# Kernel optimization log

Hardware: AMD Instinct MI355X
Metric: run time of the kernel (lower is better)

Reference implementation:

```python
import jax, jax.numpy as jnp
import numpy as np

NEG = -100000.0  # matches torch masked_fill constant

def setup_inputs() -> dict:
    key = jax.random.key(0)
    k1, k2, k3, k4 = jax.random.split(key, 4)
    B, T, D, H, S = 8, 2048, 1024, 8, 128
    features = jax.random.normal(k1, (B, T, D), dtype=jnp.float32)
    begins = jax.random.randint(k2, (B, S), 0, 2016, dtype=jnp.int64)
    widths = jax.random.randint(k3, (B, S), 1, 33, dtype=jnp.int64)
    ends = jnp.minimum(begins + widths, T)
    key_w = jax.random.normal(k4, (H, D), dtype=jnp.float32) / np.sqrt(D)
    key_b = jnp.zeros((H,), dtype=jnp.float32)
    return {"features": features, "begins": begins, "ends": ends,
            "key_w": key_w, "key_b": key_b}


def reference(features, begins, ends, key_w, key_b):
    # features: [B, T, D]; begins/ends: [B, S]
    B, T, D = features.shape
    H = key_w.shape[0]
    S = begins.shape[1]
    pos = jnp.arange(T)  # [T]
    # span mask [B, S, T]
    mask = (begins[..., None] <= pos) & (pos < ends[..., None])
    # key projection: [B, T, H]
    logits = jnp.einsum('btd,hd->bth', features, key_w) + key_b
    # masked softmax over T per (batch, span, head): [B, S, T, H]
    masked = jnp.where(mask[..., None], logits[:, None, :, :], NEG)
    weights = jax.nn.softmax(masked, axis=-2)
    # values = features reshaped to heads: [B, T, H, D//H]
    values = features.reshape(B, T, H, D // H)
    res = jnp.einsum('bthd,bsth->bshd', values, weights)  # [B, S, H, D//H]
    return res.reshape(B, S, D)
```

## Files before the change

kernel.cpp:

```cpp
#include <hip/hip_runtime.h>

#define B_  8
#define T_  2048
#define D_  1024
#define H_  8
#define S_  128
#define DH_ 128
#define MAXW 32

__global__ __launch_bounds__(256) void logits_kernel(
    const float* __restrict__ feat,
    const float* __restrict__ kw,
    const float* __restrict__ kb,
    float* __restrict__ logits)
{
    const int wave = threadIdx.x >> 6;
    const int lane = threadIdx.x & 63;
    const int row  = blockIdx.x * 4 + wave;

    const float* fr = feat + (size_t)row * D_;
    float4 f[4];
#pragma unroll
    for (int c = 0; c < 4; ++c)
        f[c] = *(const float4*)(fr + c * 256 + lane * 4);

    float acc[H_];
#pragma unroll
    for (int h = 0; h < H_; ++h) {
        const float* kr = kw + h * D_;
        float s = 0.f;
#pragma unroll
        for (int c = 0; c < 4; ++c) {
            float4 k = *(const float4*)(kr + c * 256 + lane * 4);
            s += f[c].x * k.x + f[c].y * k.y + f[c].z * k.z + f[c].w * k.w;
        }
        acc[h] = s;
    }

#pragma unroll
    for (int off = 32; off >= 1; off >>= 1) {
#pragma unroll
        for (int h = 0; h < H_; ++h)
            acc[h] += __shfl_xor(acc[h], off, 64);
    }

    if (lane == 0) {
        float4 o0 = make_float4(acc[0] + kb[0], acc[1] + kb[1],
                                acc[2] + kb[2], acc[3] + kb[3]);
        float4 o1 = make_float4(acc[4] + kb[4], acc[5] + kb[5],
                                acc[6] + kb[6], acc[7] + kb[7]);
        float4* op = (float4*)(logits + (size_t)row * H_);
        op[0] = o0;
        op[1] = o1;
    }
}

__global__ __launch_bounds__(256) void pool_kernel(
    const float* __restrict__ feat,
    const int* __restrict__ begins,
    const int* __restrict__ ends,
    const float* __restrict__ logits,
    float* __restrict__ out)
{
    const int bs  = blockIdx.x;
    const int b   = bs >> 7;
    const int tid = threadIdx.x;

    const int begin = begins[bs];
    const int end   = ends[bs];
    const int width = end - begin;

    __shared__ float lg[MAXW * H_];
    __shared__ float w [MAXW * H_];

    if (tid < width * H_)
        lg[tid] = logits[(size_t)(b * T_ + begin) * H_ + tid];
    __syncthreads();

    if (tid < H_) {
        float m = -1e30f;
        for (int i = 0; i < width; ++i) m = fmaxf(m, lg[i * H_ + tid]);
        float sum = 0.f;
        for (int i = 0; i < width; ++i) {
            float e = __expf(lg[i * H_ + tid] - m);
            w[i * H_ + tid] = e;
            sum += e;
        }
        float inv = 1.f / sum;
        for (int i = 0; i < width; ++i) w[i * H_ + tid] *= inv;
    }
    __syncthreads();

    const int col = tid * 4;
    const int hh  = tid >> 5;
    float4 acc = make_float4(0.f, 0.f, 0.f, 0.f);
    const float* fbase = feat + (size_t)(b * T_ + begin) * D_ + col;

    for (int i = 0; i < width; ++i) {
        float4 v = *(const float4*)(fbase + (size_t)i * D_);
        const float wt = w[i * H_ + hh];
        acc.x += wt * v.x;
        acc.y += wt * v.y;
        acc.z += wt * v.z;
        acc.w += wt * v.w;
    }

    *(float4*)(out + (size_t)bs * D_ + col) = acc;
}

extern "C" void kernel_launch(void* const* d_in, const int* in_sizes, int n_in,
                              void* d_out, int out_size, void* d_ws, size_t ws_size,
                              hipStream_t stream) {
    const float* feat   = (const float*)d_in[0];
    const int*   begins = (const int*)d_in[1];
    const int*   ends   = (const int*)d_in[2];
    const float* kw     = (const float*)d_in[3];
    const float* kb     = (const float*)d_in[4];
    float*       out    = (float*)d_out;
    float* logits = (float*)d_ws;

    logits_kernel<<<(B_ * T_) / 4, 256, 0, stream>>>(feat, kw, kb, logits);
    pool_kernel<<<B_ * S_, 256, 0, stream>>>(feat, begins, ends, logits, out);
}
```

Before: 126.6 us.

## Process eight rows per wave in logits kernel and warp-level softmax in pool

The logits kernel now has each wave handle eight feature rows. Key-weight vectors are loaded once per chunk and reused across those rows, and a transpose-style butterfly reduction leaves each lane holding one (row, head) result, which makes the store coalesced. The pool kernel replaces the shared-memory, single-thread-per-head softmax with wave-level shuffle reductions, drops both barriers, and reads span weights by shuffle. It also unrolls the feature accumulation loop by eight, so it reads up to seven padding rows past the span end, multiplied by zero weight. The costs are heavier register pressure (64 accumulators per lane) and possible out-of-range reads at the tail of the tensor.

```diff
diff --git a/kernel.cpp b/kernel.cpp
--- a/kernel.cpp
+++ b/kernel.cpp
@@ -5,8 +5,6 @@
 #define D_  1024
 #define H_  8
 #define S_  128
-#define DH_ 128
-#define MAXW 32
 
 __global__ __launch_bounds__(256) void logits_kernel(
     const float* __restrict__ feat,
@@ -16,43 +14,41 @@
 {
     const int wave = threadIdx.x >> 6;
     const int lane = threadIdx.x & 63;
-    const int row  = blockIdx.x * 4 + wave;
+    const int row0 = (blockIdx.x * 4 + wave) * 8;
 
-    const float* fr = feat + (size_t)row * D_;
-    float4 f[4];
+    float acc[64];
 #pragma unroll
-    for (int c = 0; c < 4; ++c)
-        f[c] = *(const float4*)(fr + c * 256 + lane * 4);
+    for (int j = 0; j < 64; ++j) acc[j] = 0.f;
 
-    float acc[H_];
 #pragma unroll
-    for (int h = 0; h < H_; ++h) {
-        const float* kr = kw + h * D_;
-        float s = 0.f;
+    for (int c = 0; c < 4; ++c) {
+        float4 kf[H_];
 #pragma unroll
-        for (int c = 0; c < 4; ++c) {
-            float4 k = *(const float4*)(kr + c * 256 + lane * 4);
-            s += f[c].x * k.x + f[c].y * k.y + f[c].z * k.z + f[c].w * k.w;
+        for (int h = 0; h < H_; ++h)
+            kf[h] = *(const float4*)(kw + h * D_ + c * 256 + lane * 4);
+#pragma unroll
+        for (int r = 0; r < 8; ++r) {
+            float4 fv = *(const float4*)(feat + (size_t)(row0 + r) * D_ + c * 256 + lane * 4);
+#pragma unroll
+            for (int h = 0; h < H_; ++h)
+                acc[r * 8 + h] += fv.x * kf[h].x + fv.y * kf[h].y
+                                + fv.z * kf[h].z + fv.w * kf[h].w;
         }
-        acc[h] = s;
     }
 
 #pragma unroll
-    for (int off = 32; off >= 1; off >>= 1) {
+    for (int s = 0; s < 6; ++s) {
+        const int m = 1 << s;
+        const bool hi = (lane >> s) & 1;
 #pragma unroll
-        for (int h = 0; h < H_; ++h)
-            acc[h] += __shfl_xor(acc[h], off, 64);
+        for (int j = 0; j < (32 >> s); ++j) {
+            float mine  = hi ? acc[2 * j + 1] : acc[2 * j];
+            float other = hi ? acc[2 * j]     : acc[2 * j + 1];
+            acc[j] = mine + __shfl_xor(other, m, 64);
+        }
     }
 
-    if (lane == 0) {
-        float4 o0 = make_float4(acc[0] + kb[0], acc[1] + kb[1],
-                                acc[2] + kb[2], acc[3] + kb[3]);
-        float4 o1 = make_float4(acc[4] + kb[4], acc[5] + kb[5],
-                                acc[6] + kb[6], acc[7] + kb[7]);
-        float4* op = (float4*)(logits + (size_t)row * H_);
-        op[0] = o0;
-        op[1] = o1;
-    }
+    logits[(size_t)row0 * H_ + lane] = acc[0] + kb[lane & 7];
 }
 
 __global__ __launch_bounds__(256) void pool_kernel(
@@ -62,50 +58,71 @@
     const float* __restrict__ logits,
     float* __restrict__ out)
 {
-    const int bs  = blockIdx.x;
-    const int b   = bs >> 7;
-    const int tid = threadIdx.x;
+    const int bs   = blockIdx.x;
+    const int wv   = threadIdx.x >> 6;
+    const int lane = threadIdx.x & 63;
+    const int b    = bs >> 7;
 
     const int begin = begins[bs];
-    const int end   = ends[bs];
-    const int width = end - begin;
+    const int width = ends[bs] - begin;
+    const size_t row0 = (size_t)b * T_ + begin;
 
-    __shared__ float lg[MAXW * H_];
-    __shared__ float w [MAXW * H_];
+    float4 lv = *(const float4*)(logits + row0 * H_ + lane * 4);
+    const int w8 = width * H_;
+    float v0 = (4 * lane + 0 < w8) ? lv.x : -1e30f;
+    float v1 = (4 * lane + 1 < w8) ? lv.y : -1e30f;
+    float v2 = (4 * lane + 2 < w8) ? lv.z : -1e30f;
+    float v3 = (4 * lane + 3 < w8) ? lv.w : -1e30f;
 
-    if (tid < width * H_)
-        lg[tid] = logits[(size_t)(b * T_ + begin) * H_ + tid];
-    __syncthreads();
-
-    if (tid < H_) {
-        float m = -1e30f;
-        for (int i = 0; i < width; ++i) m = fmaxf(m, lg[i * H_ + tid]);
-        float sum = 0.f;
-        for (int i = 0; i < width; ++i) {
-            float e = __expf(lg[i * H_ + tid] - m);
-            w[i * H_ + tid] = e;
-            sum += e;
-        }
-        float inv = 1.f / sum;
-        for (int i = 0; i < width; ++i) w[i * H_ + tid] *= inv;
-    }
-    __syncthreads();
-
-    const int col = tid * 4;
-    const int hh  = tid >> 5;
-    float4 acc = make_float4(0.f, 0.f, 0.f, 0.f);
-    const float* fbase = feat + (size_t)(b * T_ + begin) * D_ + col;
-
-    for (int i = 0; i < width; ++i) {
-        float4 v = *(const float4*)(fbase + (size_t)i * D_);
-        const float wt = w[i * H_ + hh];
-        acc.x += wt * v.x;
-        acc.y += wt * v.y;
-        acc.z += wt * v.z;
-        acc.w += wt * v.w;
+    float m0 = v0, m1 = v1, m2 = v2, m3 = v3;
+#pragma unroll
+    for (int off = 2; off <= 32; off <<= 1) {
+        m0 = fmaxf(m0, __shfl_xor(m0, off, 64));
+        m1 = fmaxf(m1, __shfl_xor(m1, off, 64));
+        m2 = fmaxf(m2, __shfl_xor(m2, off, 64));
+        m3 = fmaxf(m3, __shfl_xor(m3, off, 64));
     }
 
-    *(float4*)(out + (size_t)bs * D_ + col) = acc;
+    float e0 = __expf(v0 - m0);
+    float e1 = __expf(v1 - m1);
+    float e2 = __expf(v2 - m2);
+    float e3 = __expf(v3 - m3);
+    float s0 = e0, s1 = e1, s2 = e2, s3 = e3;
+#pragma unroll
+    for (int off = 2; off <= 32; off <<= 1) {
+        s0 += __shfl_xor(s0, off, 64);
+        s1 += __shfl_xor(s1, off, 64);
+        s2 += __shfl_xor(s2, off, 64);
+        s3 += __shfl_xor(s3, off, 64);
+    }
+    const float w0 = e0 / s0, w1 = e1 / s1, w2 = e2 / s2, w3 = e3 / s3;
+
+    const int p = wv >> 1;
+    const float wlo = (wv & 1) ? w2 : w0;
+    const float whi = (wv & 1) ? w3 : w1;
+    const bool hiHalf = (lane >= 32);
+
+    const int colbase = wv * 256 + lane * 4;
+    const float* fbase = feat + row0 * D_ + colbase;
+
+    float4 acc = make_float4(0.f, 0.f, 0.f, 0.f);
+    const int nch = (width + 7) >> 3;
+    for (int ch = 0; ch < nch; ++ch) {
+#pragma unroll
+        for (int k = 0; k < 8; ++k) {
+            const int i = ch * 8 + k;
+            const float t0 = __shfl(wlo, 2 * i + p, 64);
+            const float t1 = __shfl(whi, 2 * i + p, 64);
+            const float wt = hiHalf ? t1 : t0;
+            const float4 fv = *(const float4*)(fbase + (size_t)i * D_);
+            acc.x += wt * fv.x;
+            acc.y += wt * fv.y;
+            acc.z += wt * fv.z;
+            acc.w += wt * fv.w;
+        }
+    }
+
+    *(float4*)(out + (size_t)bs * D_ + colbase) = acc;
 }
 
 extern "C" void kernel_launch(void* const* d_in, const int* in_sizes, int n_in,
@@ -119,6 +136,6 @@
     float*       out    = (float*)d_out;
     float* logits = (float*)d_ws;
 
-    logits_kernel<<<(B_ * T_) / 4, 256, 0, stream>>>(feat, kw, kb, logits);
+    logits_kernel<<<(B_ * T_) / 32, 256, 0, stream>>>(feat, kw, kb, logits);
     pool_kernel<<<B_ * S_, 256, 0, stream>>>(feat, begins, ends, logits, out);
 }
```

Result: faster. 115.5 us (-8.8%).
